# Kernel tuning notes

Hardware: AMD Instinct MI355X
Metric: run time of the kernel (lower is better)

## Reference

```python
import jax, jax.numpy as jnp
import numpy as np
from jax.scipy.special import logsumexp

N, T, F, S, L = 16, 800, 90, 128, 200
NEG = -1e30
DEN_SCALE = 1.0


def setup_inputs() -> dict:
    key = jax.random.key(0)
    ks = jax.random.split(key, 6)
    # nnet_output is the output of log_softmax (per the docstring)
    logits = jax.random.normal(ks[0], (N, T, F), dtype=jnp.float32)
    nnet_output = jax.nn.log_softmax(logits, axis=-1)
    seq_idx = jnp.arange(N, dtype=jnp.int32)
    starts = jnp.zeros((N,), dtype=jnp.int32)
    nframes = jax.random.randint(ks[1], (N,), T // 2, T + 1).astype(jnp.int32)
    supervision_segments = jnp.stack([seq_idx, starts, nframes], axis=1)
    # shared denominator graph: dense log transition weights + state phone labels
    den_trans = jax.random.normal(ks[2], (S, S), dtype=jnp.float32) - 2.0
    den_labels = jax.random.randint(ks[3], (S,), 0, F).astype(jnp.int32)
    # numerator linear-chain graphs: per-utterance phone label sequences
    num_labels = jax.random.randint(ks[4], (N, L), 0, F).astype(jnp.int32)
    num_lens = jax.random.randint(ks[5], (N,), L // 2, L + 1).astype(jnp.int32)
    return {
        'nnet_output': nnet_output,
        'supervision_segments': supervision_segments,
        'den_trans': den_trans,
        'den_labels': den_labels,
        'num_labels': num_labels,
        'num_lens': num_lens,
    }


def _mmi_tot_scores(nnet_output, num_frames, den_trans, den_labels, num_labels, num_lens):
    """Log-semiring forward scores: num - den_scale * den per utterance."""
    x = jnp.transpose(nnet_output, (1, 0, 2))  # [T, N, F]
    ts = jnp.arange(T)

    # ---- denominator: shared dense WFSA, forward algorithm ----
    def den_step(alpha, inp):
        x_t, t = inp  # x_t: [N, F]
        emit = x_t[:, den_labels]  # [N, S] gather of frame log-probs
        new = logsumexp(alpha[:, :, None] + den_trans[None, :, :], axis=1) + emit
        alpha = jnp.where((t < num_frames)[:, None], new, alpha)
        return alpha, None

    a0 = jnp.full((N, S), NEG, dtype=nnet_output.dtype).at[:, 0].set(0.0)
    den_alpha, _ = jax.lax.scan(den_step, a0, (x, ts))
    den_scores = logsumexp(den_alpha, axis=1)  # [N]

    # ---- numerator: per-utterance linear chain (self-loop or advance) ----
    def num_step(alpha, inp):
        x_t, t = inp
        emit = jnp.take_along_axis(x_t, num_labels, axis=1)  # [N, L]
        body = jnp.logaddexp(alpha[:, 1:], alpha[:, :L]) + emit
        new = jnp.concatenate(
            [jnp.full((N, 1), NEG, dtype=alpha.dtype), body], axis=1)
        alpha = jnp.where((t < num_frames)[:, None], new, alpha)
        return alpha, None

    b0 = jnp.full((N, L + 1), NEG, dtype=nnet_output.dtype).at[:, 0].set(0.0)
    num_alpha, _ = jax.lax.scan(num_step, b0, (x, ts))
    num_scores = jnp.take_along_axis(num_alpha, num_lens[:, None], axis=1)[:, 0]

    return num_scores - DEN_SCALE * den_scores


def reference(nnet_output, supervision_segments, den_trans, den_labels, num_labels, num_lens):
    num_frames = supervision_segments[:, 2]
    tot = _mmi_tot_scores(nnet_output, num_frames, den_trans, den_labels,
                          num_labels, num_lens)
    # drop sequences whose score diverged (mirrors get_tot_objf_and_num_frames)
    finite = jnp.isfinite(tot) & (tot > 0.5 * NEG)
    tot_score = jnp.sum(jnp.where(finite, tot, 0.0))
    tot_frames = jnp.sum(jnp.where(finite, num_frames, 0))
    all_frames = jnp.sum(num_frames)
    return tot_score, tot_frames, all_frames
```

## Files before the change

### kernel.cpp

```cpp
#include <hip/hip_runtime.h>
#include <math.h>

#define NB 16
#define TT 800
#define FF 90
#define SS 128
#define LL 200
#define NEGV (-1e30f)

#define DNODES 16
#define DNDRX 50
#define QNODES 32
#define QDRX 25
#define BROW 26
#define BST 28
#define NEGH (-60000.0f)
#define EPAD 228
#define LN2F 0.69314718055994531f
#define LOG2E 1.4426950408889634f

typedef __attribute__((ext_vector_type(8))) short short8;
typedef __attribute__((ext_vector_type(4))) float float4v;
typedef _Float16 h4 __attribute__((ext_vector_type(4)));

static __device__ __forceinline__ unsigned short f2bf(float x) {
    union { float f; unsigned u; } v; v.f = x;
    unsigned r = (v.u + 0x7FFFu + ((v.u >> 16) & 1u)) >> 16;
    return (unsigned short)r;
}
static __device__ __forceinline__ unsigned packperm(float a, float b) {
    return __builtin_amdgcn_perm(__float_as_uint(b), __float_as_uint(a),
                                 0x07060302u);
}
static __device__ __forceinline__ int xsw(int row, int wrd) {
    return (wrd & 3) | ((((wrd >> 2) ^ (row & 7)) << 2));
}

__global__ __launch_bounds__(512, 2) void mmi_nodes(
    const float* __restrict__ x,
    const int*   __restrict__ sup,
    const float* __restrict__ trans,
    const int*   __restrict__ den_labels,
    const int*   __restrict__ num_labels,
    unsigned*    __restrict__ Pout,
    float*       __restrict__ scales8,
    _Float16*    __restrict__ Bd)
{
    __shared__ __align__(16) unsigned char SMEM[58368];
    const int tid = threadIdx.x;

    if (blockIdx.x < NB * DNODES) {
        const int bid = blockIdx.x;
        const int u  = bid >> 4;
        const int nd = bid & 15;
        const int t0 = nd * DNDRX;
        const int nf = sup[u * 3 + 2];
        unsigned* Pg = Pout + (size_t)bid * 8192;

        if (t0 >= nf) {
            #pragma unroll
            for (int k2 = 0; k2 < 16; ++k2) {
                const int ww = tid + k2 * 512;
                const int row = ww >> 6, colw = ww & 63;
                unsigned val = 0;
                if (row == 2 * colw)     val |= 0x3F80u;
                if (row == 2 * colw + 1) val |= 0x3F800000u;
                Pg[ww] = val;
            }
            if (tid < 8) scales8[bid * 8 + tid] = 0.0f;
            return;
        }

        const int w = tid >> 6, l = tid & 63;
        const int m15 = l & 15, q = l >> 4, h = m15 & 7;

        unsigned* AFs = (unsigned*)SMEM;
        #pragma unroll
        for (int i = 0; i < 16; ++i) {
            const int wi = tid + i * 512;
            const int f  = wi >> 2, j2 = wi & 3;
            const int fl = f & 63, kc = (f >> 6) & 3, mt = f >> 8;
            const int col = mt * 16 + (fl & 15);
            const int krow = kc * 32 + (fl >> 4) * 8 + 2 * j2;
            const float a = __expf(trans[(krow    ) * SS + col]);
            const float b = __expf(trans[(krow + 1) * SS + col]);
            AFs[wi] = (unsigned)f2bf(a) | ((unsigned)f2bf(b) << 16);
        }
        __syncthreads();
        short8 afrag[8][4];
        #pragma unroll
        for (int mt = 0; mt < 8; ++mt)
            #pragma unroll
            for (int kc = 0; kc < 4; ++kc)
                afrag[mt][kc] =
                    *(const short8*)(AFs + ((mt * 4 + kc) * 64 + l) * 4);
        __syncthreads();

        unsigned* Xs  = (unsigned*)SMEM;
        float* ptab   = (float*)(SMEM + 32768);

        for (int idx = tid; idx < DNDRX * SS; idx += 512) {
            const int tt = idx >> 7, d = idx & 127;
            const int fr = min(t0 + tt, TT - 1);
            ptab[idx] = __expf(x[((size_t)u * TT + fr) * FF + den_labels[d]]);
        }
        __syncthreads();

        unsigned* Xw = Xs + w * (16 * 64);
        {
            const float p0 = ptab[2 * l], p1 = ptab[2 * l + 1];
            #pragma unroll
            for (int k2 = 0; k2 < 16; ++k2) {
                const int R = w * 16 + k2;
                const float2 t2 = ((const float2*)trans)[R * 64 + l];
                Xw[k2 * 64 + xsw(k2, l)] = packperm(__expf(t2.x) * p0,
                                                    __expf(t2.y) * p1);
            }
        }

        const unsigned short* XwH = (const unsigned short*)Xw;
        const int kmax = min(DNDRX, nf - t0);
        int eacc = 0;
        float redmax = 1.0f;

        for (int k = 1; k < kmax; ++k) {
            const bool dosc = ((k & 3) == 0);
            float sc = 1.0f;
            if (dosc) {
                const float mm = fmaxf(redmax, 1e-37f);
                const int e = (int)((__float_as_uint(mm) >> 23) & 255u);
                sc = __uint_as_float((unsigned)(254 - e) << 23);
                eacc += (e - 127);
            }

            short8 bf[4];
            #pragma unroll
            for (int kc = 0; kc < 4; ++kc)
                bf[kc] = *(const short8*)(XwH + m15 * 128 +
                                          8 * (((kc << 2) | q) ^ h));

            float4v acc[8];
            #pragma unroll
            for (int mt = 0; mt < 8; ++mt) {
                float4v z = {0.f, 0.f, 0.f, 0.f};
                acc[mt] = z;
            }
            __builtin_amdgcn_s_setprio(1);
            #pragma unroll
            for (int kc = 0; kc < 4; ++kc)
                #pragma unroll
                for (int mt = 0; mt < 8; ++mt)
                    acc[mt] = __builtin_amdgcn_mfma_f32_16x16x32_bf16(
                        afrag[mt][kc], bf[kc], acc[mt], 0, 0, 0);
            __builtin_amdgcn_s_setprio(0);

            const bool dmax = ((k & 3) == 3);
            float vmax = 0.0f;
            #pragma unroll
            for (int mt = 0; mt < 8; ++mt) {
                float4 pc = *(const float4*)(ptab + k * SS + mt * 16 + 4 * q);
                if (dosc) { pc.x *= sc; pc.y *= sc; pc.z *= sc; pc.w *= sc; }
                acc[mt][0] *= pc.x;
                acc[mt][1] *= pc.y;
                acc[mt][2] *= pc.z;
                acc[mt][3] *= pc.w;
                if (dmax)
                    vmax = fmaxf(vmax,
                        fmaxf(fmaxf(acc[mt][0], acc[mt][1]),
                              fmaxf(acc[mt][2], acc[mt][3])));
            }
            if (dmax) {
                #pragma unroll
                for (int off = 32; off >= 1; off >>= 1)
                    vmax = fmaxf(vmax, __shfl_xor(vmax, off, 64));
                redmax = vmax;
            }

            #pragma unroll
            for (int mt = 0; mt < 8; ++mt) {
                uint2 pk;
                pk.x = packperm(acc[mt][0], acc[mt][1]);
                pk.y = packperm(acc[mt][2], acc[mt][3]);
                *(uint2*)(Xw + m15 * 64 +
                          4 * (((mt << 1) | (q >> 1)) ^ h) + 2 * (q & 1)) = pk;
            }
        }

        #pragma unroll
        for (int k2 = 0; k2 < 16; ++k2)
            Pg[(w * 16 + k2) * 64 + l] = Xw[k2 * 64 + xsw(k2, l)];
        if (l == 0) scales8[bid * 8 + w] = (float)eacc;
        return;
    }

    {
        float* est = (float*)(SMEM + 16);

        const int qb    = blockIdx.x - NB * DNODES;
        const int slot0 = qb * 2;
        const int u     = slot0 / QNODES;
        const int nd0   = slot0 - u * QNODES;
        const int nf    = sup[u * 3 + 2];
        const int* nlu  = num_labels + u * LL;

        for (int idx = tid; idx < 2 * QDRX * EPAD; idx += 512) {
            const int g   = idx / (QDRX * EPAD);
            const int rem = idx - g * (QDRX * EPAD);
            const int tt  = rem / EPAD;
            const int j   = rem - tt * EPAD;
            const int jj  = min(j, 199);
            const int fr  = min((nd0 + g) * QDRX + tt, TT - 1);
            est[idx] = x[((size_t)u * TT + fr) * FF + nlu[jj]] * LOG2E;
        }
        __syncthreads();

        const int g  = tid >> 8;
        const int c  = tid & 255;
        const int nd = nd0 + g;
        const int t0 = nd * QDRX;
        const int kmaxg = min(QDRX, max(nf - t0, 0));
        const float* eg = est + g * (QDRX * EPAD);

        float a[BROW];
        a[0] = 0.0f;
        #pragma unroll
        for (int d = 1; d < BROW; ++d) a[d] = NEGV;

        const float* etc = eg + (c - 1);
        for (int t = 0; t < kmaxg; ++t, etc += EPAD) {
            const int tc = t + 1;
            #pragma unroll
            for (int d = BROW - 1; d >= 1; --d) {
                if (d <= tc) {
                    const float e  = etc[d];
                    const float aa = a[d], bb = a[d - 1];
                    const float mx = fmaxf(aa, bb);
                    const float dd = fminf(aa, bb) - mx;
                    a[d] = e + mx +
                           __builtin_amdgcn_logf(
                               1.0f + __builtin_amdgcn_exp2f(dd));
                }
            }
            a[0] = (c == 0) ? NEGV : (etc[0] + a[0]);
        }

        if (c <= 200) {
            _Float16* Bg = Bd + (size_t)(slot0 + g) * 201 * BST;
            #pragma unroll
            for (int d = 0; d < BROW; ++d) {
                const int r = c + d;
                if (r <= 200) Bg[r * BST + d] = (_Float16)fmaxf(a[d], NEGH);
            }
            if (c < BROW - 1) {
                for (int kk = c + 1; kk < BROW; ++kk)
                    Bg[c * BST + kk] = (_Float16)NEGH;
            }
        }
    }
}

__global__ __launch_bounds__(512) void mmi_chain(
    const unsigned short* __restrict__ Pmat,
    const _Float16* __restrict__ Bd,
    const float* __restrict__ scales8,
    const int* __restrict__ num_lens,
    const int* __restrict__ sup,
    float* __restrict__ dsc,
    int*   __restrict__ ctr,
    float* __restrict__ out)
{
    __shared__ float sh_v[SS];
    __shared__ float sh_part[16 * SS];
    __shared__ float sh_red[2];
    __shared__ float ab[2][232];
    __shared__ int sfl;

    const int tid = threadIdx.x;

    if (blockIdx.x < NB) {
        const int u = blockIdx.x;
        const int gg = tid & 31, c = tid >> 5;
        const unsigned short* Pu = Pmat + (size_t)u * DNODES * 16384;

        if (tid < SS) sh_v[tid] = (tid == 0) ? 1.0f : 0.0f;
        int   e2acc = 0;
        float sscal = 0.0f;

        uint2 cur[8], nx1[8], nx2[8];
        #pragma unroll
        for (int j = 0; j < 8; ++j)
            cur[j] = *(const uint2*)(Pu + (8 * c + j) * SS + 4 * gg);
        #pragma unroll
        for (int j = 0; j < 8; ++j)
            nx1[j] = *(const uint2*)(Pu + 16384 + (8 * c + j) * SS + 4 * gg);
        __syncthreads();

        for (int i = 0; i < DNODES; ++i) {
            if (i + 2 < DNODES) {
                const unsigned short* Pn = Pu + (size_t)(i + 2) * 16384;
                #pragma unroll
                for (int j = 0; j < 8; ++j)
                    nx2[j] = *(const uint2*)(Pn + (8 * c + j) * SS + 4 * gg);
            }
            const float* s8 = scales8 + (size_t)(u * DNODES + i) * 8;
            float gmax = s8[0];
            #pragma unroll
            for (int g2 = 1; g2 < 8; ++g2) gmax = fmaxf(gmax, s8[g2]);
            const float fgr = __builtin_amdgcn_exp2f(s8[c >> 1] - gmax);
            sscal += gmax;

            const float4* av = (const float4*)(sh_v + 8 * c);
            float4 aa[2] = {av[0], av[1]};
            const float* as = (const float*)aa;
            float4 acc = make_float4(0.f, 0.f, 0.f, 0.f);
            #pragma unroll
            for (int j = 0; j < 8; ++j) {
                const float e0 = __uint_as_float(cur[j].x << 16);
                const float e1 = __uint_as_float(cur[j].x & 0xFFFF0000u);
                const float e2 = __uint_as_float(cur[j].y << 16);
                const float e3 = __uint_as_float(cur[j].y & 0xFFFF0000u);
                acc.x = fmaf(as[j], e0, acc.x);
                acc.y = fmaf(as[j], e1, acc.y);
                acc.z = fmaf(as[j], e2, acc.z);
                acc.w = fmaf(as[j], e3, acc.w);
            }
            acc.x *= fgr; acc.y *= fgr; acc.z *= fgr; acc.w *= fgr;
            *(float4*)(sh_part + c * SS + 4 * gg) = acc;
            __syncthreads();

            float v = 0.0f;
            if (tid < SS) {
                float y = 0.0f;
                #pragma unroll
                for (int cc = 0; cc < 16; ++cc) y += sh_part[cc * SS + tid];
                v = y;
                float m = v;
                #pragma unroll
                for (int off = 32; off >= 1; off >>= 1)
                    m = fmaxf(m, __shfl_xor(m, off, 64));
                if ((tid & 63) == 0) sh_red[tid >> 6] = m;
            }
            __syncthreads();
            if (tid < SS) {
                const float mm = fmaxf(fmaxf(sh_red[0], sh_red[1]), 1e-37f);
                const int e = (int)((__float_as_uint(mm) >> 23) & 255u);
                const float inv = __uint_as_float((unsigned)(254 - e) << 23);
                e2acc += (e - 127);
                sh_v[tid] = v * inv;
            }
            #pragma unroll
            for (int j = 0; j < 8; ++j) { cur[j] = nx1[j]; nx1[j] = nx2[j]; }
            __syncthreads();
        }

        if (tid < SS) {
            float s = sh_v[tid];
            #pragma unroll
            for (int off = 32; off >= 1; off >>= 1)
                s += __shfl_xor(s, off, 64);
            if ((tid & 63) == 0) sh_red[tid >> 6] = s;
        }
        __syncthreads();
        if (tid == 0)
            atomicExch(&dsc[u], LN2F * ((float)e2acc + sscal) +
                                __logf(sh_red[0] + sh_red[1]));
    } else {
        const int u = blockIdx.x - NB;
        const _Float16* Bu = Bd + (size_t)u * QNODES * 201 * BST;
        const int r = tid;
        const bool act = (r < 201);

        if (r < 232) { ab[0][r] = NEGV; ab[1][r] = NEGV; }
        h4 nx1[7], nx2[7];
        float dv[BROW];
        if (act) {
            const h4* s0 = (const h4*)(Bu + (size_t)r * BST);
            #pragma unroll
            for (int t7 = 0; t7 < 7; ++t7) nx1[t7] = s0[t7];
            #pragma unroll
            for (int k = 0; k < BROW; ++k) dv[k] = (float)nx1[k >> 2][k & 3];
            const h4* s1 = (const h4*)(Bu + ((size_t)201 + r) * BST);
            #pragma unroll
            for (int t7 = 0; t7 < 7; ++t7) nx1[t7] = s1[t7];
        }
        __syncthreads();
        if (r == 0) ab[0][QDRX] = 0.0f;
        __syncthreads();

        int cur = 0;
        for (int nd = 0; nd < QNODES; ++nd) {
            if (nd + 2 < QNODES && act) {
                const h4* src = (const h4*)(Bu + ((size_t)(nd + 2) * 201 + r) * BST);
                #pragma unroll
                for (int t7 = 0; t7 < 7; ++t7) nx2[t7] = src[t7];
            }
            float anew = NEGV;
            if (act) {
                float tr[BROW];
                #pragma unroll
                for (int k = 0; k < BROW; ++k)
                    tr[k] = dv[k] + ab[cur][QDRX + r - k];
                float m = tr[0];
                #pragma unroll
                for (int k = 1; k < BROW; ++k) m = fmaxf(m, tr[k]);
                float s = 0.0f;
                #pragma unroll
                for (int k = 0; k < BROW; ++k)
                    s += __builtin_amdgcn_exp2f(tr[k] - m);
                anew = m + __builtin_amdgcn_logf(s);
            }
            if (act) ab[cur ^ 1][QDRX + r] = anew;
            cur ^= 1;
            __syncthreads();
            if (act) {
                #pragma unroll
                for (int k = 0; k < BROW; ++k) dv[k] = (float)nx1[k >> 2][k & 3];
                #pragma unroll
                for (int t7 = 0; t7 < 7; ++t7) nx1[t7] = nx2[t7];
            }
        }
        if (r == 0)
            atomicExch(&dsc[NB + u], ab[cur][QDRX + num_lens[u]] * LN2F);
    }

    __threadfence();
    if (tid == 0) sfl = (atomicAdd(ctr, 1) == 2 * NB - 1);
    __syncthreads();
    if (!sfl) return;
    __threadfence();
    if (tid < 64) {
        float tot_score = 0.0f, tot_frames = 0.0f, all_frames = 0.0f;
        if (tid < NB) {
            const float d = atomicAdd(&dsc[tid], 0.0f);
            const float n = atomicAdd(&dsc[NB + tid], 0.0f);
            const float tot = n - d;
            const int nf = sup[tid * 3 + 2];
            const bool fin = isfinite(tot) && (tot > 0.5f * NEGV);
            tot_score  = fin ? tot : 0.0f;
            tot_frames = fin ? (float)nf : 0.0f;
            all_frames = (float)nf;
        }
        #pragma unroll
        for (int off = 32; off >= 1; off >>= 1) {
            tot_score  += __shfl_xor(tot_score, off, 64);
            tot_frames += __shfl_xor(tot_frames, off, 64);
            all_frames += __shfl_xor(all_frames, off, 64);
        }
        if (tid == 0) {
            out[0] = tot_score;
            out[1] = tot_frames;
            out[2] = all_frames;
        }
    }
}

__global__ void mmi_finalize(const float* __restrict__ sc,
                             const int* __restrict__ sup,
                             float* __restrict__ out)
{
    const int tid = threadIdx.x;
    float tot_score = 0.0f, tot_frames = 0.0f, all_frames = 0.0f;
    if (tid < NB) {
        const float tot = sc[NB + tid] - sc[tid];
        const int nf = sup[tid * 3 + 2];
        const bool fin = isfinite(tot) && (tot > 0.5f * NEGV);
        tot_score  = fin ? tot : 0.0f;
        tot_frames = fin ? (float)nf : 0.0f;
        all_frames = (float)nf;
    }
    #pragma unroll
    for (int off = 32; off >= 1; off >>= 1) {
        tot_score  += __shfl_xor(tot_score, off, 64);
        tot_frames += __shfl_xor(tot_frames, off, 64);
        all_frames += __shfl_xor(all_frames, off, 64);
    }
    if (tid == 0) {
        out[0] = tot_score;
        out[1] = tot_frames;
        out[2] = all_frames;
    }
}

#define XBF (16 * FF)
__global__ __launch_bounds__(256) void mmi_forward_fb(
    const float* __restrict__ x, const int* __restrict__ sup,
    const float* __restrict__ trans, const int* __restrict__ den_labels,
    const int* __restrict__ num_labels, const int* __restrict__ num_lens,
    float* __restrict__ ws)
{
    const int tid = threadIdx.x;
    if (blockIdx.x < NB) {
        __shared__ float sh_v[SS];
        __shared__ float sh_part[8 * SS];
        __shared__ float sh_red[4];
        __shared__ __align__(16) float xbuf[2][XBF];
        const int n = blockIdx.x, nf = sup[n * 3 + 2];
        const int g = tid & 31, c = tid >> 5;
        float4 e[16];
        #pragma unroll
        for (int j = 0; j < 16; ++j) {
            const float4 t4 = *(const float4*)(trans + (size_t)(16 * c + j) * SS + 4 * g);
            e[j] = make_float4(__expf(t4.x), __expf(t4.y), __expf(t4.z), __expf(t4.w));
        }
        const int lab = (tid < SS) ? den_labels[tid & (SS - 1)] : 0;
        const float* xb = x + (size_t)n * TT * FF;
        {
            const float4* s0 = (const float4*)xb;
            float4 p0 = s0[tid]; float4 p1; if (tid < 104) p1 = s0[256 + tid];
            float4* d0 = (float4*)xbuf[0];
            d0[tid] = p0; if (tid < 104) d0[256 + tid] = p1;
        }
        if (tid < SS) sh_v[tid] = (tid == 0) ? 1.0f : 0.0f;
        float logM = 0.0f, v = 0.0f, pe = 0.0f;
        float4 pf0, pf1;
        __syncthreads();
        for (int t = 0; t < nf; ++t) {
            const int b = t >> 4;
            if (tid < SS) pe = __expf(xbuf[b & 1][(t & 15) * FF + lab]);
            float4 aa[4];
            { const float4* av = (const float4*)(sh_v + 16 * c);
              aa[0] = av[0]; aa[1] = av[1]; aa[2] = av[2]; aa[3] = av[3]; }
            const float* as = (const float*)aa;
            float4 acc = make_float4(0.f, 0.f, 0.f, 0.f);
            #pragma unroll
            for (int j = 0; j < 16; ++j) {
                acc.x = fmaf(as[j], e[j].x, acc.x); acc.y = fmaf(as[j], e[j].y, acc.y);
                acc.z = fmaf(as[j], e[j].z, acc.z); acc.w = fmaf(as[j], e[j].w, acc.w);
            }
            *(float4*)(sh_part + c * SS + 4 * g) = acc;
            if ((t & 15) == 8) {
                const int tn = (b + 1) * 16;
                if (tn < nf) {
                    const float4* s = (const float4*)(xb + (size_t)tn * FF);
                    pf0 = s[tid]; if (tid < 104) pf1 = s[256 + tid];
                }
            }
            __syncthreads();
            const bool rs = ((t & 15) == 15);
            if (tid < SS) {
                float y = 0.0f;
                #pragma unroll
                for (int cc = 0; cc < 8; ++cc) y += sh_part[cc * SS + tid];
                v = y * pe;
                if (rs) {
                    float m = v;
                    #pragma unroll
                    for (int off = 32; off >= 1; off >>= 1)
                        m = fmaxf(m, __shfl_xor(m, off, 64));
                    if ((tid & 63) == 0) sh_red[tid >> 6] = m;
                }
            }
            if (rs) {
                const int tn = (b + 1) * 16;
                if (tn < nf) {
                    float4* dst = (float4*)xbuf[(b + 1) & 1];
                    dst[tid] = pf0; if (tid < 104) dst[256 + tid] = pf1;
                }
                __syncthreads();
                if (tid < SS) {
                    float mm = fmaxf(fmaxf(sh_red[0], sh_red[1]), 1e-37f);
                    v *= (1.0f / mm); logM += __logf(mm);
                }
            }
            if (tid < SS) sh_v[tid] = v;
            __syncthreads();
        }
        if (tid < SS) {
            float ssum = v;
            #pragma unroll
            for (int off = 32; off >= 1; off >>= 1) ssum += __shfl_xor(ssum, off, 64);
            if ((tid & 63) == 0) sh_red[2 + (tid >> 6)] = ssum;
        }
        __syncthreads();
        if (tid == 0) ws[n] = logM + __logf(sh_red[2] + sh_red[3]);
    } else {
        const int w = tid >> 6, l = tid & 63;
        const int n = (blockIdx.x - NB) * 4 + w;
        const int nf = sup[n * 3 + 2];
        const float* xb = x + (size_t)n * TT * FF;
        const int* nl = num_labels + n * LL;
        int li[4];
        #pragma unroll
        for (int k = 0; k < 4; ++k) li[k] = nl[min(4 * l + k, LL - 1)];
        float a4[4] = {NEGV, NEGV, NEGV, NEGV};
        float ea[4], eb[4];
        #pragma unroll
        for (int k = 0; k < 4; ++k) ea[k] = xb[li[k]];
        { const float* xr = xb + (size_t)min(1, nf - 1) * FF;
          #pragma unroll
          for (int k = 0; k < 4; ++k) eb[k] = xr[li[k]]; }
        auto step = [&](float (&ee)[4], int t) {
            float left = __shfl_up(a4[3], 1, 64);
            if (l == 0) left = (t == 0) ? 0.0f : NEGV;
            float prev = left;
            #pragma unroll
            for (int k = 0; k < 4; ++k) {
                const float a = a4[k], b = prev;
                const float mx = fmaxf(a, b), mn = fminf(a, b);
                const float nv = mx + __logf(1.0f + __expf(mn - mx)) + ee[k];
                prev = a4[k]; a4[k] = nv;
            }
            const int t2 = min(t + 2, nf - 1);
            const float* xr = xb + (size_t)t2 * FF;
            #pragma unroll
            for (int k = 0; k < 4; ++k) ee[k] = xr[li[k]];
        };
        int t = 0;
        while (t < nf) { step(ea, t); ++t; if (t >= nf) break; step(eb, t); ++t; }
        const int idx = num_lens[n] - 1;
        if ((idx >> 2) == l) {
            const int kk = idx & 3;
            float vv = (kk == 0) ? a4[0] : (kk == 1) ? a4[1] : (kk == 2) ? a4[2] : a4[3];
            ws[NB + n] = vv;
        }
    }
}

extern "C" void kernel_launch(void* const* d_in, const int* in_sizes, int n_in,
                              void* d_out, int out_size, void* d_ws, size_t ws_size,
                              hipStream_t stream) {
    const float* x          = (const float*)d_in[0];
    const int*   sup        = (const int*)d_in[1];
    const float* trans      = (const float*)d_in[2];
    const int*   den_labels = (const int*)d_in[3];
    const int*   num_labels = (const int*)d_in[4];
    const int*   num_lens   = (const int*)d_in[5];
    float* out = (float*)d_out;

    const size_t PBYTES = (size_t)NB * DNODES * 32768;
    const size_t BBYTES = (size_t)NB * QNODES * 201 * BST * 2;
    const size_t SCB    = (size_t)NB * DNODES * 8 * sizeof(float);
    const size_t SOFF   = PBYTES + BBYTES;
    const size_t DOFF   = SOFF + SCB;
    const size_t COFF   = DOFF + 256;
    const size_t NEEDED = COFF + 256;

    if (ws_size >= NEEDED) {
        unsigned*  Pout    = (unsigned*)d_ws;
        _Float16*  Bd      = (_Float16*)((char*)d_ws + PBYTES);
        float*     scales8 = (float*)((char*)d_ws + SOFF);
        float*     dsc     = (float*)((char*)d_ws + DOFF);
        int*       ctr     = (int*)((char*)d_ws + COFF);
        hipMemsetAsync(ctr, 0, 64, stream);
        mmi_nodes<<<dim3(512), dim3(512), 0, stream>>>(
            x, sup, trans, den_labels, num_labels, Pout, scales8, Bd);
        mmi_chain<<<dim3(2 * NB), dim3(512), 0, stream>>>(
            (const unsigned short*)d_ws, Bd, scales8, num_lens, sup,
            dsc, ctr, out);
    } else {
        float* ws = (float*)d_ws;
        mmi_forward_fb<<<dim3(20), dim3(256), 0, stream>>>(
            x, sup, trans, den_labels, num_labels, num_lens, ws);
        mmi_finalize<<<dim3(1), dim3(64), 0, stream>>>(ws, sup, out);
    }
}
```

Baseline: 197.2 us.

## Pack emission table as bf16, halve chain block size, drop counter memset

The per-frame emission table in the node kernel is now stored as packed bf16 pairs in a layout matched to the MFMA accumulator fragment. This shrinks shared memory and lets each lane fetch its scale factors with wide loads. The denominator chain kernel runs with 256 threads, so each thread handles 16 rows of the transition matrix with single-stage prefetch, and the partial-sum reduction shrinks to 8 slices. The memset of the completion counter is removed: the last block is now detected by checking the counter modulo 32, which assumes the workspace counter starts aligned to a multiple of 32. The bf16 emission table also lowers precision.

```diff
diff --git a/kernel.cpp b/kernel.cpp
--- a/kernel.cpp
+++ b/kernel.cpp
@@ -46,7 +46,7 @@
     float*       __restrict__ scales8,
     _Float16*    __restrict__ Bd)
 {
-    __shared__ __align__(16) unsigned char SMEM[58368];
+    __shared__ __align__(16) unsigned char SMEM[45632];
     const int tid = threadIdx.x;
 
     if (blockIdx.x < NB * DNODES) {
@@ -96,19 +96,27 @@
                     *(const short8*)(AFs + ((mt * 4 + kc) * 64 + l) * 4);
         __syncthreads();
 
-        unsigned* Xs  = (unsigned*)SMEM;
-        float* ptab   = (float*)(SMEM + 32768);
-
-        for (int idx = tid; idx < DNDRX * SS; idx += 512) {
-            const int tt = idx >> 7, d = idx & 127;
-            const int fr = min(t0 + tt, TT - 1);
-            ptab[idx] = __expf(x[((size_t)u * TT + fr) * FF + den_labels[d]]);
+        unsigned* Xs    = (unsigned*)SMEM;
+        unsigned* ptabH = (unsigned*)(SMEM + 32768);
+
+        for (int idx = tid; idx < DNDRX * 64; idx += 512) {
+            const int k = idx >> 6, r = idx & 63;
+            const int q2 = r >> 4, mtt = r & 15;
+            const int pr = (mtt >> 1) * 8 + 2 * q2 + (mtt & 1);
+            const int fr = min(t0 + k, TT - 1);
+            const float* xr = x + ((size_t)u * TT + fr) * FF;
+            const float ea = __expf(xr[den_labels[2 * pr]]);
+            const float eb = __expf(xr[den_labels[2 * pr + 1]]);
+            ptabH[idx] = (unsigned)f2bf(ea) | ((unsigned)f2bf(eb) << 16);
         }
         __syncthreads();
 
         unsigned* Xw = Xs + w * (16 * 64);
         {
-            const float p0 = ptab[2 * l], p1 = ptab[2 * l + 1];
+            const unsigned pp = ptabH[((l & 7) >> 1) * 16 + (l >> 3) * 2 +
+                                      (l & 1)];
+            const float p0 = __uint_as_float(pp << 16);
+            const float p1 = __uint_as_float(pp & 0xFFFF0000u);
             #pragma unroll
             for (int k2 = 0; k2 < 16; ++k2) {
                 const int R = w * 16 + k2;
@@ -156,18 +164,38 @@
 
             const bool dmax = ((k & 3) == 3);
             float vmax = 0.0f;
-            #pragma unroll
-            for (int mt = 0; mt < 8; ++mt) {
-                float4 pc = *(const float4*)(ptab + k * SS + mt * 16 + 4 * q);
-                if (dosc) { pc.x *= sc; pc.y *= sc; pc.z *= sc; pc.w *= sc; }
-                acc[mt][0] *= pc.x;
-                acc[mt][1] *= pc.y;
-                acc[mt][2] *= pc.z;
-                acc[mt][3] *= pc.w;
-                if (dmax)
+            const unsigned* pcb = ptabH + k * 64 + q * 16;
+            #pragma unroll
+            for (int i = 0; i < 4; ++i) {
+                const uint4 pu = *(const uint4*)(pcb + 4 * i);
+                float f0 = __uint_as_float(pu.x << 16);
+                float f1 = __uint_as_float(pu.x & 0xFFFF0000u);
+                float f2 = __uint_as_float(pu.y << 16);
+                float f3 = __uint_as_float(pu.y & 0xFFFF0000u);
+                float f4 = __uint_as_float(pu.z << 16);
+                float f5 = __uint_as_float(pu.z & 0xFFFF0000u);
+                float f6 = __uint_as_float(pu.w << 16);
+                float f7 = __uint_as_float(pu.w & 0xFFFF0000u);
+                if (dosc) {
+                    f0 *= sc; f1 *= sc; f2 *= sc; f3 *= sc;
+                    f4 *= sc; f5 *= sc; f6 *= sc; f7 *= sc;
+                }
+                acc[2 * i][0] *= f0;
+                acc[2 * i][1] *= f1;
+                acc[2 * i][2] *= f2;
+                acc[2 * i][3] *= f3;
+                acc[2 * i + 1][0] *= f4;
+                acc[2 * i + 1][1] *= f5;
+                acc[2 * i + 1][2] *= f6;
+                acc[2 * i + 1][3] *= f7;
+                if (dmax) {
                     vmax = fmaxf(vmax,
-                        fmaxf(fmaxf(acc[mt][0], acc[mt][1]),
-                              fmaxf(acc[mt][2], acc[mt][3])));
+                        fmaxf(fmaxf(acc[2 * i][0], acc[2 * i][1]),
+                              fmaxf(acc[2 * i][2], acc[2 * i][3])));
+                    vmax = fmaxf(vmax,
+                        fmaxf(fmaxf(acc[2 * i + 1][0], acc[2 * i + 1][1]),
+                              fmaxf(acc[2 * i + 1][2], acc[2 * i + 1][3])));
+                }
             }
             if (dmax) {
                 #pragma unroll
@@ -259,18 +287,18 @@
     }
 }
 
-__global__ __launch_bounds__(512) void mmi_chain(
+__global__ __launch_bounds__(256) void mmi_chain(
     const unsigned short* __restrict__ Pmat,
     const _Float16* __restrict__ Bd,
     const float* __restrict__ scales8,
     const int* __restrict__ num_lens,
     const int* __restrict__ sup,
     float* __restrict__ dsc,
-    int*   __restrict__ ctr,
+    unsigned* __restrict__ ctr,
     float* __restrict__ out)
 {
     __shared__ float sh_v[SS];
-    __shared__ float sh_part[16 * SS];
+    __shared__ float sh_part[8 * SS];
     __shared__ float sh_red[2];
     __shared__ float ab[2][232];
     __shared__ int sfl;
@@ -286,39 +314,36 @@
         int   e2acc = 0;
         float sscal = 0.0f;
 
-        uint2 cur[8], nx1[8], nx2[8];
-        #pragma unroll
-        for (int j = 0; j < 8; ++j)
-            cur[j] = *(const uint2*)(Pu + (8 * c + j) * SS + 4 * gg);
-        #pragma unroll
-        for (int j = 0; j < 8; ++j)
-            nx1[j] = *(const uint2*)(Pu + 16384 + (8 * c + j) * SS + 4 * gg);
+        uint2 curm[16], nxt[16];
+        #pragma unroll
+        for (int j = 0; j < 16; ++j)
+            curm[j] = *(const uint2*)(Pu + (16 * c + j) * SS + 4 * gg);
         __syncthreads();
 
         for (int i = 0; i < DNODES; ++i) {
-            if (i + 2 < DNODES) {
-                const unsigned short* Pn = Pu + (size_t)(i + 2) * 16384;
-                #pragma unroll
-                for (int j = 0; j < 8; ++j)
-                    nx2[j] = *(const uint2*)(Pn + (8 * c + j) * SS + 4 * gg);
+            if (i + 1 < DNODES) {
+                const unsigned short* Pn = Pu + (size_t)(i + 1) * 16384;
+                #pragma unroll
+                for (int j = 0; j < 16; ++j)
+                    nxt[j] = *(const uint2*)(Pn + (16 * c + j) * SS + 4 * gg);
             }
             const float* s8 = scales8 + (size_t)(u * DNODES + i) * 8;
             float gmax = s8[0];
             #pragma unroll
             for (int g2 = 1; g2 < 8; ++g2) gmax = fmaxf(gmax, s8[g2]);
-            const float fgr = __builtin_amdgcn_exp2f(s8[c >> 1] - gmax);
+            const float fgr = __builtin_amdgcn_exp2f(s8[c] - gmax);
             sscal += gmax;
 
-            const float4* av = (const float4*)(sh_v + 8 * c);
-            float4 aa[2] = {av[0], av[1]};
+            const float4* av = (const float4*)(sh_v + 16 * c);
+            float4 aa[4] = {av[0], av[1], av[2], av[3]};
             const float* as = (const float*)aa;
             float4 acc = make_float4(0.f, 0.f, 0.f, 0.f);
             #pragma unroll
-            for (int j = 0; j < 8; ++j) {
-                const float e0 = __uint_as_float(cur[j].x << 16);
-                const float e1 = __uint_as_float(cur[j].x & 0xFFFF0000u);
-                const float e2 = __uint_as_float(cur[j].y << 16);
-                const float e3 = __uint_as_float(cur[j].y & 0xFFFF0000u);
+            for (int j = 0; j < 16; ++j) {
+                const float e0 = __uint_as_float(curm[j].x << 16);
+                const float e1 = __uint_as_float(curm[j].x & 0xFFFF0000u);
+                const float e2 = __uint_as_float(curm[j].y << 16);
+                const float e3 = __uint_as_float(curm[j].y & 0xFFFF0000u);
                 acc.x = fmaf(as[j], e0, acc.x);
                 acc.y = fmaf(as[j], e1, acc.y);
                 acc.z = fmaf(as[j], e2, acc.z);
@@ -332,7 +357,7 @@
             if (tid < SS) {
                 float y = 0.0f;
                 #pragma unroll
-                for (int cc = 0; cc < 16; ++cc) y += sh_part[cc * SS + tid];
+                for (int cc = 0; cc < 8; ++cc) y += sh_part[cc * SS + tid];
                 v = y;
                 float m = v;
                 #pragma unroll
@@ -349,7 +374,7 @@
                 sh_v[tid] = v * inv;
             }
             #pragma unroll
-            for (int j = 0; j < 8; ++j) { cur[j] = nx1[j]; nx1[j] = nx2[j]; }
+            for (int j = 0; j < 16; ++j) curm[j] = nxt[j];
             __syncthreads();
         }
 
@@ -424,7 +449,7 @@
     }
 
     __threadfence();
-    if (tid == 0) sfl = (atomicAdd(ctr, 1) == 2 * NB - 1);
+    if (tid == 0) sfl = ((atomicAdd(ctr, 1u) & 31u) == 31u);
     __syncthreads();
     if (!sfl) return;
     __threadfence();
@@ -640,11 +665,10 @@
         _Float16*  Bd      = (_Float16*)((char*)d_ws + PBYTES);
         float*     scales8 = (float*)((char*)d_ws + SOFF);
         float*     dsc     = (float*)((char*)d_ws + DOFF);
-        int*       ctr     = (int*)((char*)d_ws + COFF);
-        hipMemsetAsync(ctr, 0, 64, stream);
+        unsigned*  ctr     = (unsigned*)((char*)d_ws + COFF);
         mmi_nodes<<<dim3(512), dim3(512), 0, stream>>>(
             x, sup, trans, den_labels, num_labels, Pout, scales8, Bd);
-        mmi_chain<<<dim3(2 * NB), dim3(512), 0, stream>>>(
+        mmi_chain<<<dim3(2 * NB), dim3(256), 0, stream>>>(
             (const unsigned short*)d_ws, Bd, scales8, num_lens, sup,
             dsc, ctr, out);
     } else {
```

Result: faster. 175.4 us (-11.0%).
